# Kernel optimization log

Hardware: AMD Instinct MI355X
Metric: run time of the kernel (lower is better)

Reference implementation:

```python
import jax, jax.numpy as jnp
import numpy as np

DIM = 1024
N_HEAD = 16
HEAD_DIM = DIM // N_HEAD
B, T = 2, 2048


def setup_inputs() -> dict:
    key = jax.random.key(0)
    ks = jax.random.split(key, 9)
    s = 1.0 / np.sqrt(DIM)
    return {
        "x": jax.random.normal(ks[0], (B, T, DIM), dtype=jnp.float32),
        "Wq": jax.random.normal(ks[1], (DIM, DIM), dtype=jnp.float32) * s,
        "bq": jax.random.normal(ks[2], (DIM,), dtype=jnp.float32) * s,
        "Wk": jax.random.normal(ks[3], (DIM, DIM), dtype=jnp.float32) * s,
        "bk": jax.random.normal(ks[4], (DIM,), dtype=jnp.float32) * s,
        "Wv": jax.random.normal(ks[5], (DIM, DIM), dtype=jnp.float32) * s,
        "bv": jax.random.normal(ks[6], (DIM,), dtype=jnp.float32) * s,
        "Wo": jax.random.normal(ks[7], (DIM, DIM), dtype=jnp.float32) * s,
        "bo": jax.random.normal(ks[8], (DIM,), dtype=jnp.float32) * s,
    }


def reference(x, Wq, bq, Wk, bk, Wv, bv, Wo, bo):
    b, t, d = x.shape
    # torch nn.Linear: y = x @ W.T + b
    Q = x @ Wq.T + bq  # [b, t, d]
    K = x @ Wk.T + bk
    V = x @ Wv.T + bv
    # split heads -> [b, h, t, hd]
    Q = Q.reshape(b, t, N_HEAD, HEAD_DIM).transpose(0, 2, 1, 3)
    K = K.reshape(b, t, N_HEAD, HEAD_DIM).transpose(0, 2, 1, 3)
    V = V.reshape(b, t, N_HEAD, HEAD_DIM).transpose(0, 2, 1, 3)
    scale = 1.0 / jnp.sqrt(jnp.float32(HEAD_DIM))
    score = jnp.einsum('bhqd,bhkd->bhqk', Q, K) * scale  # [b, h, t, t]
    attn = jax.nn.softmax(score, axis=-1)
    # dropout is identity in eval mode
    out = jnp.einsum('bhqk,bhkd->bhqd', attn, V)  # [b, h, t, hd]
    out = out.transpose(0, 2, 1, 3).reshape(b, t, d)
    return out @ Wo.T + bo
```

## Files before the change

### kernel.cpp

```cpp
#include <hip/hip_runtime.h>


#define DIM 1024
#define NH 16
#define HD 64
#define SEQ 2048
#define NROWS 4096
#define NT 32

typedef unsigned short u16;
typedef unsigned int u32;
typedef __bf16 bf16_t;
typedef bf16_t bf16x8 __attribute__((ext_vector_type(8)));
typedef float f32x4 __attribute__((ext_vector_type(4)));
typedef u16 u16x4 __attribute__((ext_vector_type(4)));
typedef u32 u32x4 __attribute__((ext_vector_type(4)));

typedef const __attribute__((address_space(1))) void* gas_ptr;
typedef __attribute__((address_space(3))) void* las_ptr;

#define S_BARRIER() asm volatile("s_barrier" ::: "memory")
#define S_WAITCNT_VM(N) asm volatile("s_waitcnt vmcnt(" #N ")" ::: "memory")

__device__ __forceinline__ void gl_lds16(const void* g, void* lds_wave_base) {
  __builtin_amdgcn_global_load_lds((gas_ptr)g, (las_ptr)lds_wave_base, 16, 0, 0);
}

__device__ __forceinline__ f32x4 mfma_bf16(bf16x8 a, bf16x8 b, f32x4 c) {
  return __builtin_amdgcn_mfma_f32_16x16x32_bf16(a, b, c, 0, 0, 0);
}

__device__ __forceinline__ u32 cvtpk(float lo, float hi) {
  u32 r;
  asm("v_cvt_pk_bf16_f32 %0, %1, %2" : "=v"(r) : "v"(lo), "v"(hi));
  return r;
}

__device__ __forceinline__ u16 bfu(float f) {
  bf16_t b = (bf16_t)f;
  union { bf16_t b; u16 u; } cv; cv.b = b; return cv.u;
}

__device__ __forceinline__ float fexp2(float x) {
#if __has_builtin(__builtin_amdgcn_exp2f)
  return __builtin_amdgcn_exp2f(x);
#else
  return exp2f(x);
#endif
}

#define QSCALE 0.18033688f

__global__ void cvt_all(const float* __restrict__ x,
                        const float* __restrict__ wq, const float* __restrict__ wk,
                        const float* __restrict__ wv, const float* __restrict__ wo,
                        u16* __restrict__ xb,
                        u16* __restrict__ oq, u16* __restrict__ ok,
                        u16* __restrict__ ov, u16* __restrict__ oo) {
  const int bid = blockIdx.x;
  const float* in;
  u16* out;
  float s = 1.0f;
  int off;
  if (bid < 4096) {
    in = x; out = xb; off = bid;
  } else {
    const int wi = (bid - 4096) >> 10;
    off = (bid - 4096) & 1023;
    in = wi == 0 ? wq : wi == 1 ? wk : wi == 2 ? wv : wo;
    out = wi == 0 ? oq : wi == 1 ? ok : wi == 2 ? ov : oo;
    if (wi == 0) s = QSCALE;
  }
  const int i = off * 256 + threadIdx.x;
  float4 v = ((const float4*)in)[i];
  u16x4 o;
  o.x = bfu(v.x * s); o.y = bfu(v.y * s); o.z = bfu(v.z * s); o.w = bfu(v.w * s);
  ((u16x4*)out)[i] = o;
}

__global__ __launch_bounds__(256, 3) void gemm_qkv(const u16* __restrict__ A,
                                                   const u16* __restrict__ wq,
                                                   const u16* __restrict__ wk,
                                                   const u16* __restrict__ wv,
                                                   const float* __restrict__ bq,
                                                   const float* __restrict__ bk,
                                                   const float* __restrict__ bv,
                                                   u16* __restrict__ Qb,
                                                   u16* __restrict__ Kb,
                                                   u16* __restrict__ Vtb) {
  __shared__ u16 As[3][128 * 32];
  __shared__ u16 Bs[3][128 * 32];
  const int L = blockIdx.y * gridDim.x + blockIdx.x;
  const int bx = (L >> 3) % 24;
  const int by = (L / 192) * 8 + (L & 7);
  const int which = bx >> 3;
  const int col0 = (bx & 7) * 128;
  const u16* W = which == 0 ? wq : which == 1 ? wk : wv;
  const float* bias = which == 0 ? bq : which == 1 ? bk : bv;
  const float bscale = which == 0 ? QSCALE : 1.0f;

  const int t = threadIdx.x, lane = t & 63, w = t >> 6;
  const int row0 = by * 128;
  const int wr = w >> 1, wc = w & 1;
  const int lr = lane & 15, lk = lane >> 4;

  f32x4 acc[4][4] = {};

  auto stage = [&](int k0, int bu) {
#pragma unroll
    for (int i = 0; i < 2; ++i) {
      const int bc = i * 256 + w * 64;
      const int f = bc + lane;
      gl_lds16(A + (size_t)(row0 + (f >> 2)) * DIM + k0 + (f & 3) * 8, &As[bu][bc * 8]);
      gl_lds16(W + (size_t)(col0 + (f >> 2)) * DIM + k0 + (f & 3) * 8, &Bs[bu][bc * 8]);
    }
  };

  stage(0, 0);
  stage(32, 1);
  int bcur = 0, bst = 2;
  for (int k = 0; k < 32; ++k) {
    S_BARRIER();
    if (k + 2 < 32) { stage((k + 2) * 32, bst); S_WAITCNT_VM(8); }
    else if (k + 1 < 32) { S_WAITCNT_VM(4); }
    else { S_WAITCNT_VM(0); }
    S_BARRIER();

    bf16x8 a[4], b[4];
#pragma unroll
    for (int m = 0; m < 4; ++m)
      a[m] = *(const bf16x8*)&As[bcur][(wr * 64 + m * 16 + lr) * 32 + lk * 8];
#pragma unroll
    for (int n = 0; n < 4; ++n)
      b[n] = *(const bf16x8*)&Bs[bcur][(wc * 64 + n * 16 + lr) * 32 + lk * 8];
    __builtin_amdgcn_s_setprio(1);
#pragma unroll
    for (int m = 0; m < 4; ++m)
#pragma unroll
      for (int n = 0; n < 4; ++n)
        acc[m][n] = mfma_bf16(a[m], b[n], acc[m][n]);
    __builtin_amdgcn_s_setprio(0);

    bcur = bcur == 2 ? 0 : bcur + 1;
    bst = bst == 2 ? 0 : bst + 1;
  }

#pragma unroll
  for (int m = 0; m < 4; ++m) {
    const int rowb = row0 + wr * 64 + m * 16 + lk * 4;
#pragma unroll
    for (int n = 0; n < 4; ++n) {
      const int ocol = col0 + wc * 64 + n * 16 + lr;
      const float bc = bias[ocol] * bscale;
      if (which != 2) {
        u16* dst = which == 0 ? Qb : Kb;
#pragma unroll
        for (int r = 0; r < 4; ++r)
          dst[(size_t)(rowb + r) * DIM + ocol] = bfu(acc[m][n][r] + bc);
      } else {
        u16x4 pk;
#pragma unroll
        for (int r = 0; r < 4; ++r) pk[r] = bfu(acc[m][n][r] + bc);
        const int tin = rowb & 2047;
        const int vlo = tin & 63;
        const int kap = (vlo & 32) | ((vlo & 12) << 1) | ((vlo & 16) >> 2) | (vlo & 3);
        const int tperm = (tin & ~63) | kap;
        const size_t idx = ((((size_t)(rowb >> 11) * NH + (ocol >> 6)) * HD + (ocol & 63)) << 11) + tperm;
        *(u16x4*)&Vtb[idx] = pk;
      }
    }
  }
}

__global__ __launch_bounds__(256, 2) void gemm_out(const u16* __restrict__ A,
                                                   const u16* __restrict__ W,
                                                   const float* __restrict__ bias,
                                                   float* __restrict__ C) {
  __shared__ u16 As[3][64 * 32];
  __shared__ u16 Bs[3][128 * 32];
  const int L = blockIdx.x;
  const int bx = (L >> 3) & 7;
  const int by = (L >> 6) * 8 + (L & 7);
  const int row0 = by * 64, col0 = bx * 128;
  const int t = threadIdx.x, lane = t & 63, w = t >> 6;
  const int wr = w >> 1, wc = w & 1;
  const int lr = lane & 15, lk = lane >> 4;

  f32x4 acc[2][4] = {};

  auto stage = [&](int k0, int bu) {
    const int fa = w * 64 + lane;
    gl_lds16(A + (size_t)(row0 + (fa >> 2)) * DIM + k0 + (fa & 3) * 8, &As[bu][w * 512]);
#pragma unroll
    for (int i = 0; i < 2; ++i) {
      const int bc = i * 256 + w * 64;
      const int fb = bc + lane;
      gl_lds16(W + (size_t)(col0 + (fb >> 2)) * DIM + k0 + (fb & 3) * 8, &Bs[bu][bc * 8]);
    }
  };

  stage(0, 0);
  stage(32, 1);
  int bcur = 0, bst = 2;
  for (int k = 0; k < 32; ++k) {
    S_BARRIER();
    if (k + 2 < 32) { stage((k + 2) * 32, bst); S_WAITCNT_VM(6); }
    else if (k + 1 < 32) { S_WAITCNT_VM(3); }
    else { S_WAITCNT_VM(0); }
    S_BARRIER();

    bf16x8 a[2], b[4];
#pragma unroll
    for (int m = 0; m < 2; ++m)
      a[m] = *(const bf16x8*)&As[bcur][(wr * 32 + m * 16 + lr) * 32 + lk * 8];
#pragma unroll
    for (int n = 0; n < 4; ++n)
      b[n] = *(const bf16x8*)&Bs[bcur][(wc * 64 + n * 16 + lr) * 32 + lk * 8];
    __builtin_amdgcn_s_setprio(1);
#pragma unroll
    for (int m = 0; m < 2; ++m)
#pragma unroll
      for (int n = 0; n < 4; ++n)
        acc[m][n] = mfma_bf16(a[m], b[n], acc[m][n]);
    __builtin_amdgcn_s_setprio(0);

    bcur = bcur == 2 ? 0 : bcur + 1;
    bst = bst == 2 ? 0 : bst + 1;
  }

#pragma unroll
  for (int m = 0; m < 2; ++m) {
    const int rowb = row0 + wr * 32 + m * 16 + lk * 4;
#pragma unroll
    for (int n = 0; n < 4; ++n) {
      const int col = col0 + wc * 64 + n * 16 + lr;
      const float bc = bias[col];
#pragma unroll
      for (int r = 0; r < 4; ++r)
        C[(size_t)(rowb + r) * DIM + col] = acc[m][n][r] + bc;
    }
  }
}

__global__ __launch_bounds__(256, 5) void flash_attn(const u16* __restrict__ Q,
                                                     const u16* __restrict__ K,
                                                     const u16* __restrict__ Vt,
                                                     u16* __restrict__ O) {
  __shared__ u16 Ks[2][64 * 64];
  __shared__ u16 Vs[2][64 * 64];

  const int t = threadIdx.x, lane = t & 63, w = t >> 6;
  const int L = blockIdx.x;
  const int bh = ((L >> 8) << 3) | (L & 7);
  const int qt = (L >> 3) & 31;
  const int b = bh >> 4, h = bh & 15;
  const int q0 = qt * 64;
  const int lr = lane & 15, lk = lane >> 4;

  const size_t qrow = (size_t)(b * SEQ + q0 + w * 16 + lr);
  bf16x8 qf[2];
  qf[0] = *(const bf16x8*)&Q[qrow * DIM + h * HD + lk * 8];
  qf[1] = *(const bf16x8*)&Q[qrow * DIM + h * HD + lk * 8 + 32];

  bf16x8 ones;
#pragma unroll
  for (int j = 0; j < 8; ++j) ones[j] = (bf16_t)1.0f;

  f32x4 o[4] = {};
  f32x4 lacc = {};

  auto stage = [&](int kt, int bu) {
#pragma unroll
    for (int i = 0; i < 2; ++i) {
      const int bc = i * 256 + w * 64;
      const int f = bc + lane;
      const int row = f >> 3, c = f & 7;
      const int cs = c ^ (row & 7);
      gl_lds16(K + (size_t)(b * SEQ + kt + row) * DIM + h * HD + cs * 8, &Ks[bu][bc * 8]);
      gl_lds16(Vt + (((size_t)bh * HD + row) << 11) + kt + cs * 8, &Vs[bu][bc * 8]);
    }
  };

  stage(0, 0);
  int buf = 0;
  for (int kt = 0; kt < SEQ; kt += 64) {
    if (kt + 64 < SEQ) { stage(kt + 64, buf ^ 1); S_WAITCNT_VM(4); }
    else               { S_WAITCNT_VM(0); }
    S_BARRIER();

    const u16* ks = Ks[buf];
    const u16* vs = Vs[buf];

    f32x4 s[4] = {};
    __builtin_amdgcn_s_setprio(1);
#pragma unroll
    for (int n = 0; n < 4; ++n) {
      const int row = n * 16 + lr;
#pragma unroll
      for (int kk = 0; kk < 2; ++kk) {
        bf16x8 kf = *(const bf16x8*)&ks[row * 64 + (((lk + kk * 4) ^ (row & 7)) * 8)];
        s[n] = mfma_bf16(kf, qf[kk], s[n]);
      }
    }
    __builtin_amdgcn_s_setprio(0);

    u32 pk[4][2];
#pragma unroll
    for (int n = 0; n < 4; ++n) {
      pk[n][0] = cvtpk(fexp2(s[n][0]), fexp2(s[n][1]));
      pk[n][1] = cvtpk(fexp2(s[n][2]), fexp2(s[n][3]));
    }

    __builtin_amdgcn_s_setprio(1);
#pragma unroll
    for (int kk = 0; kk < 2; ++kk) {
      u32x4 paw;
      paw[0] = pk[2 * kk][0]; paw[1] = pk[2 * kk][1];
      paw[2] = pk[2 * kk + 1][0]; paw[3] = pk[2 * kk + 1][1];
      bf16x8 pa = __builtin_bit_cast(bf16x8, paw);
      lacc = mfma_bf16(pa, ones, lacc);
#pragma unroll
      for (int nd = 0; nd < 4; ++nd) {
        const int vrow = nd * 16 + lr;
        bf16x8 vf = *(const bf16x8*)&vs[vrow * 64 + (((lk + kk * 4) ^ (vrow & 7)) * 8)];
        o[nd] = mfma_bf16(pa, vf, o[nd]);
      }
    }
    __builtin_amdgcn_s_setprio(0);

    S_BARRIER();
    buf ^= 1;
  }

#pragma unroll
  for (int r = 0; r < 4; ++r) {
    const float inv = 1.f / lacc[r];
    const size_t grow = (size_t)(b * SEQ + q0 + w * 16 + lk * 4 + r);
#pragma unroll
    for (int nd = 0; nd < 4; ++nd)
      O[grow * DIM + h * HD + nd * 16 + lr] = bfu(o[nd][r] * inv);
  }
}

extern "C" void kernel_launch(void* const* d_in, const int* in_sizes, int n_in,
                              void* d_out, int out_size, void* d_ws, size_t ws_size,
                              hipStream_t stream) {
  (void)in_sizes; (void)n_in; (void)out_size; (void)ws_size;
  const float* x  = (const float*)d_in[0];
  const float* Wq = (const float*)d_in[1];
  const float* bq = (const float*)d_in[2];
  const float* Wk = (const float*)d_in[3];
  const float* bk = (const float*)d_in[4];
  const float* Wv = (const float*)d_in[5];
  const float* bv = (const float*)d_in[6];
  const float* Wo = (const float*)d_in[7];
  const float* bo = (const float*)d_in[8];

  char* ws = (char*)d_ws;
  u16* xb  = (u16*)(ws + 0);
  u16* wqb = (u16*)(ws + 8388608);
  u16* wkb = (u16*)(ws + 10485760);
  u16* wvb = (u16*)(ws + 12582912);
  u16* wob = (u16*)(ws + 14680064);
  u16* Qb  = (u16*)(ws + 16777216);
  u16* Kb  = (u16*)(ws + 25165824);
  u16* Vtb = (u16*)(ws + 33554432);
  u16* Ob  = (u16*)(ws + 41943040);

  cvt_all<<<8192, 256, 0, stream>>>(x, Wq, Wk, Wv, Wo, xb, wqb, wkb, wvb, wob);

  gemm_qkv<<<dim3(24, NROWS / 128), 256, 0, stream>>>(xb, wqb, wkb, wvb, bq, bk, bv, Qb, Kb, Vtb);

  flash_attn<<<1024, 256, 0, stream>>>(Qb, Kb, Vtb, Ob);

  gemm_out<<<512, 256, 0, stream>>>(Ob, wob, bo, (float*)d_out);
}
```

Before: 115.5 us.

## Split attention along the key axis into two halves with a combine kernel

The flash attention kernel now runs twice as many blocks, each covering half of the key sequence. Each block writes unnormalized partial outputs in bf16 and row sums to workspace buffers. A new combine kernel adds the two partials, normalizes by the summed denominators and writes the head-interleaved output. The aim is more parallelism and better load balance across CUs, at the cost of an extra launch, extra memory traffic, and some precision loss from storing unnormalized partials in bf16.

After: 120.3 us. +4.2%, slower.

```diff
diff --git a/kernel.cpp b/kernel.cpp
--- a/kernel.cpp
+++ b/kernel.cpp
@@ -6,7 +6,6 @@
 #define HD 64
 #define SEQ 2048
 #define NROWS 4096
-#define NT 32
 
 typedef unsigned short u16;
 typedef unsigned int u32;
@@ -39,6 +38,10 @@
 __device__ __forceinline__ u16 bfu(float f) {
   bf16_t b = (bf16_t)f;
   union { bf16_t b; u16 u; } cv; cv.b = b; return cv.u;
+}
+
+__device__ __forceinline__ float b2f(u16 u) {
+  union { u32 u; float f; } cv; cv.u = ((u32)u) << 16; return cv.f;
 }
 
 __device__ __forceinline__ float fexp2(float x) {
@@ -242,17 +245,21 @@
   }
 }
 
-__global__ __launch_bounds__(256, 5) void flash_attn(const u16* __restrict__ Q,
-                                                     const u16* __restrict__ K,
-                                                     const u16* __restrict__ Vt,
-                                                     u16* __restrict__ O) {
+__global__ __launch_bounds__(256, 5) void flash_split(const u16* __restrict__ Q,
+                                                      const u16* __restrict__ K,
+                                                      const u16* __restrict__ Vt,
+                                                      u16* __restrict__ Op0,
+                                                      u16* __restrict__ Op1,
+                                                      float* __restrict__ Lp0,
+                                                      float* __restrict__ Lp1) {
   __shared__ u16 Ks[2][64 * 64];
   __shared__ u16 Vs[2][64 * 64];
 
   const int t = threadIdx.x, lane = t & 63, w = t >> 6;
   const int L = blockIdx.x;
-  const int bh = ((L >> 8) << 3) | (L & 7);
-  const int qt = (L >> 3) & 31;
+  const int bh = ((L >> 9) << 3) | (L & 7);
+  const int inner = (L >> 3) & 63;
+  const int qt = inner >> 1, half = inner & 1;
   const int b = bh >> 4, h = bh & 15;
   const int q0 = qt * 64;
   const int lr = lane & 15, lk = lane >> 4;
@@ -268,6 +275,9 @@
 
   f32x4 o[4] = {};
   f32x4 lacc = {};
+
+  const int kbase = half * (SEQ / 2);
+  const int kend = kbase + SEQ / 2;
 
   auto stage = [&](int kt, int bu) {
 #pragma unroll
@@ -281,11 +291,11 @@
     }
   };
 
-  stage(0, 0);
+  stage(kbase, 0);
   int buf = 0;
-  for (int kt = 0; kt < SEQ; kt += 64) {
-    if (kt + 64 < SEQ) { stage(kt + 64, buf ^ 1); S_WAITCNT_VM(4); }
-    else               { S_WAITCNT_VM(0); }
+  for (int kt = kbase; kt < kend; kt += 64) {
+    if (kt + 64 < kend) { stage(kt + 64, buf ^ 1); S_WAITCNT_VM(4); }
+    else                { S_WAITCNT_VM(0); }
     S_BARRIER();
 
     const u16* ks = Ks[buf];
@@ -332,14 +342,44 @@
     buf ^= 1;
   }
 
+  u16* Op = half ? Op1 : Op0;
+  float* Lp = half ? Lp1 : Lp0;
 #pragma unroll
   for (int r = 0; r < 4; ++r) {
-    const float inv = 1.f / lacc[r];
-    const size_t grow = (size_t)(b * SEQ + q0 + w * 16 + lk * 4 + r);
+    const size_t prow = (size_t)bh * SEQ + q0 + w * 16 + lk * 4 + r;
 #pragma unroll
     for (int nd = 0; nd < 4; ++nd)
-      O[grow * DIM + h * HD + nd * 16 + lr] = bfu(o[nd][r] * inv);
-  }
+      Op[prow * HD + nd * 16 + lr] = bfu(o[nd][r]);
+  }
+  if (lr == 0) {
+#pragma unroll
+    for (int r = 0; r < 4; ++r)
+      Lp[(size_t)bh * SEQ + q0 + w * 16 + lk * 4 + r] = lacc[r];
+  }
+}
+
+__global__ __launch_bounds__(256) void combine(const u16* __restrict__ Op0,
+                                               const u16* __restrict__ Op1,
+                                               const float* __restrict__ Lp0,
+                                               const float* __restrict__ Lp1,
+                                               u16* __restrict__ Ob) {
+  const int t = threadIdx.x;
+  const int bh = blockIdx.y;
+  const int q = blockIdx.x * 16 + (t >> 4);
+  const int d0 = (t & 15) * 4;
+  const int b = bh >> 4, hh = bh & 15;
+
+  const size_t lidx = ((size_t)bh << 11) + q;
+  const float inv = 1.f / (Lp0[lidx] + Lp1[lidx]);
+
+  const size_t base = lidx * HD + d0;
+  const u16x4 v0 = *(const u16x4*)&Op0[base];
+  const u16x4 v1 = *(const u16x4*)&Op1[base];
+  u16x4 ov;
+#pragma unroll
+  for (int j = 0; j < 4; ++j)
+    ov[j] = bfu((b2f(v0[j]) + b2f(v1[j])) * inv);
+  *(u16x4*)&Ob[(size_t)(b * SEQ + q) * DIM + hh * HD + d0] = ov;
 }
 
 extern "C" void kernel_launch(void* const* d_in, const int* in_sizes, int n_in,
@@ -366,12 +406,17 @@
   u16* Kb  = (u16*)(ws + 25165824);
   u16* Vtb = (u16*)(ws + 33554432);
   u16* Ob  = (u16*)(ws + 41943040);
+  u16*   Op0 = (u16*)(ws + 0);
+  float* Lp0 = (float*)(ws + 8388608);
+  float* Lp1 = (float*)(ws + 8650752);
+  u16*   Op1 = (u16*)(ws + 50331648);
 
   cvt_all<<<8192, 256, 0, stream>>>(x, Wq, Wk, Wv, Wo, xb, wqb, wkb, wvb, wob);
 
   gemm_qkv<<<dim3(24, NROWS / 128), 256, 0, stream>>>(xb, wqb, wkb, wvb, bq, bk, bv, Qb, Kb, Vtb);
 
-  flash_attn<<<1024, 256, 0, stream>>>(Qb, Kb, Vtb, Ob);
+  flash_split<<<2048, 256, 0, stream>>>(Qb, Kb, Vtb, Op0, Op1, Lp0, Lp1);
+  combine<<<dim3(SEQ / 16, 2 * NH), 256, 0, stream>>>(Op0, Op1, Lp0, Lp1, Ob);
 
   gemm_out<<<512, 256, 0, stream>>>(Ob, wob, bo, (float*)d_out);
 }
```
